# Performance work log

Measured on AMD Instinct MI355X. Metric: run time of the kernel, lower is better.

## Reference

```python
import jax, jax.numpy as jnp
import numpy as np

D_IN = 1024
D_OUT = 1024
NUM_HEADS = 16
HEAD_DIM = D_OUT // NUM_HEADS


def setup_inputs() -> dict:
    key = jax.random.key(0)
    k_x, k_q, k_k, k_v, k_o = jax.random.split(key, 5)
    # Xavier-uniform-ish init for weights (stored as [d_in, d_out] for x @ W)
    lim = float(np.sqrt(6.0 / (D_IN + D_OUT)) / np.sqrt(2.0))
    lim_o = float(np.sqrt(6.0 / (D_OUT + D_OUT)))
    return {
        "x": jax.random.normal(k_x, (2, 2048, D_IN), dtype=jnp.float32),
        "W_query": jax.random.uniform(k_q, (D_IN, D_OUT), jnp.float32, -lim, lim),
        "W_key": jax.random.uniform(k_k, (D_IN, D_OUT), jnp.float32, -lim, lim),
        "W_value": jax.random.uniform(k_v, (D_IN, D_OUT), jnp.float32, -lim, lim),
        "W_out": jax.random.uniform(k_o, (D_OUT, D_OUT), jnp.float32, -lim_o, lim_o),
        "b_out": jnp.zeros((D_OUT,), dtype=jnp.float32),
    }


def reference(x, W_query, W_key, W_value, W_out, b_out):
    B, S, _ = x.shape
    scale = 1.0 / np.sqrt(HEAD_DIM)

    def split_heads(t):  # [B,S,D] -> [B,H,S,hd]
        return t.reshape(B, S, NUM_HEADS, HEAD_DIM).transpose(0, 2, 1, 3)

    q = split_heads(x @ W_query)
    k = split_heads(x @ W_key)
    v = split_heads(x @ W_value)

    scores = jnp.einsum("bhqd,bhkd->bhqk", q, k) * scale  # [B,H,S,S]
    causal = jnp.tril(jnp.ones((S, S), dtype=bool))  # True = keep
    scores = jnp.where(causal, scores, -jnp.inf)
    weights = jax.nn.softmax(scores, axis=-1)
    ctx = jnp.einsum("bhqk,bhkd->bhqd", weights, v)
    ctx = ctx.transpose(0, 2, 1, 3).reshape(B, S, D_OUT)
    return ctx @ W_out + b_out
```

## Files before the change

### kernel.cpp

```cpp
#include <hip/hip_runtime.h>
#include <hip/hip_bf16.h>


typedef __bf16 bf16_t;
typedef __bf16 bf16x4 __attribute__((ext_vector_type(4)));
typedef __bf16 bf16x8 __attribute__((ext_vector_type(8)));
typedef float f32x4 __attribute__((ext_vector_type(4)));

#define AS_GLOBAL __attribute__((address_space(1)))
#define AS_LDS    __attribute__((address_space(3)))

__device__ __forceinline__ void async_load16(const void* g, void* l) {
    __builtin_amdgcn_global_load_lds((AS_GLOBAL void*)(g), (AS_LDS void*)(l), 16, 0, 0);
}

__global__ __launch_bounds__(256) void cvt_f32_bf16(const float* __restrict__ src,
                                                    bf16_t* __restrict__ dst, int n4) {
    int i = blockIdx.x * 256 + threadIdx.x;
    if (i < n4) {
        float4 v = ((const float4*)src)[i];
        bf16x4 o;
        o[0] = (bf16_t)v.x; o[1] = (bf16_t)v.y; o[2] = (bf16_t)v.z; o[3] = (bf16_t)v.w;
        ((bf16x4*)dst)[i] = o;
    }
}

__global__ __launch_bounds__(256) void transpose_cvt4(
    const float* __restrict__ W0, const float* __restrict__ W1,
    const float* __restrict__ W2, const float* __restrict__ W3,
    bf16_t* __restrict__ outbase) {
    __shared__ bf16_t T[64][65];
    int t = threadIdx.x;
    int k0 = blockIdx.x * 64, n0 = blockIdx.y * 64, z = blockIdx.z;
    const float* W = (z == 0) ? W0 : (z == 1) ? W1 : (z == 2) ? W2 : W3;
    bf16_t* WT = outbase + (size_t)z * 1048576;
#pragma unroll
    for (int c = 0; c < 4; c++) {
        int idx = c * 256 + t;
        int row = idx >> 4;
        int col4 = (idx & 15) * 4;
        float4 v = *(const float4*)(W + (k0 + row) * 1024 + n0 + col4);
        T[row][col4 + 0] = (bf16_t)v.x;
        T[row][col4 + 1] = (bf16_t)v.y;
        T[row][col4 + 2] = (bf16_t)v.z;
        T[row][col4 + 3] = (bf16_t)v.w;
    }
    __syncthreads();
#pragma unroll
    for (int c = 0; c < 4; c++) {
        int idx = c * 256 + t;
        int nrow = idx >> 4;
        int kc4 = (idx & 15) * 4;
        bf16x4 o;
        o[0] = T[kc4 + 0][nrow];
        o[1] = T[kc4 + 1][nrow];
        o[2] = T[kc4 + 2][nrow];
        o[3] = T[kc4 + 3][nrow];
        *(bf16x4*)(WT + (n0 + nrow) * 1024 + k0 + kc4) = o;
    }
}

__global__ __launch_bounds__(256) void qkv_gemm(
    const bf16_t* __restrict__ A,
    const bf16_t* __restrict__ WqT, const bf16_t* __restrict__ WkT,
    const bf16_t* __restrict__ WvT,
    bf16_t* __restrict__ Qo, bf16_t* __restrict__ Ko, bf16_t* __restrict__ Vo) {
    const int KD = 1024;
    __shared__ bf16_t As[128 * 32];
    __shared__ bf16_t Bs[128 * 32];
    int tid = threadIdx.x;
    int wave = tid >> 6, lane = tid & 63;
    int quad = lane >> 4, l16 = lane & 15;
    int wm = wave >> 1, wn = wave & 1;
    int z = blockIdx.z;
    const bf16_t* BT = (z == 0) ? WqT : (z == 1) ? WkT : WvT;
    int m0 = blockIdx.x * 128;
    int n0 = blockIdx.y * 128;

    int r = tid >> 2;
    int c8 = (tid & 3) * 8;
    const bf16_t* gA0 = A + (size_t)(m0 + r) * KD + c8;
    const bf16_t* gA1 = A + (size_t)(m0 + 64 + r) * KD + c8;
    const bf16_t* gB0 = BT + (size_t)(n0 + r) * KD + c8;
    const bf16_t* gB1 = BT + (size_t)(n0 + 64 + r) * KD + c8;
    bf16_t* lA0 = As + wave * 512;
    bf16_t* lA1 = As + 2048 + wave * 512;
    bf16_t* lB0 = Bs + wave * 512;
    bf16_t* lB1 = Bs + 2048 + wave * 512;

    f32x4 acc[4][4];
#pragma unroll
    for (int i = 0; i < 4; i++)
#pragma unroll
        for (int j = 0; j < 4; j++) acc[i][j] = (f32x4){0.f, 0.f, 0.f, 0.f};

    for (int k0 = 0; k0 < KD; k0 += 32) {
        async_load16(gA0 + k0, lA0);
        async_load16(gA1 + k0, lA1);
        async_load16(gB0 + k0, lB0);
        async_load16(gB1 + k0, lB1);
        __syncthreads();
        bf16x8 af[4], bfr[4];
#pragma unroll
        for (int mt = 0; mt < 4; mt++)
            af[mt] = *(const bf16x8*)(As + (wm * 64 + mt * 16 + l16) * 32 + quad * 8);
#pragma unroll
        for (int nt = 0; nt < 4; nt++)
            bfr[nt] = *(const bf16x8*)(Bs + (wn * 64 + nt * 16 + l16) * 32 + quad * 8);
        if (z == 2) {
#pragma unroll
            for (int mt = 0; mt < 4; mt++)
#pragma unroll
                for (int nt = 0; nt < 4; nt++)
                    acc[mt][nt] = __builtin_amdgcn_mfma_f32_16x16x32_bf16(
                        bfr[nt], af[mt], acc[mt][nt], 0, 0, 0);
        } else {
#pragma unroll
            for (int mt = 0; mt < 4; mt++)
#pragma unroll
                for (int nt = 0; nt < 4; nt++)
                    acc[mt][nt] = __builtin_amdgcn_mfma_f32_16x16x32_bf16(
                        af[mt], bfr[nt], acc[mt][nt], 0, 0, 0);
        }
        __syncthreads();
    }

    if (z == 0) {
#pragma unroll
        for (int mt = 0; mt < 4; mt++) {
            int mg_base = m0 + wm * 64 + mt * 16 + quad * 4;
#pragma unroll
            for (int nt = 0; nt < 4; nt++) {
                int ng = n0 + wn * 64 + nt * 16 + l16;
                int h = ng >> 6, d = ng & 63;
#pragma unroll
                for (int rr = 0; rr < 4; rr++) {
                    int mg = mg_base + rr;
                    int b = mg >> 11, s = mg & 2047;
                    Qo[(((size_t)(b * 16 + h) * 2048) + s) * 64 + d] =
                        (bf16_t)acc[mt][nt][rr];
                }
            }
        }
    } else if (z == 1) {
#pragma unroll
        for (int mt = 0; mt < 4; mt++) {
            int mg_base = m0 + wm * 64 + mt * 16 + quad * 4;
#pragma unroll
            for (int nt = 0; nt < 4; nt++) {
                int ng = n0 + wn * 64 + nt * 16 + l16;
                int h = ng >> 6, dd = ng & 63;
#pragma unroll
                for (int rr = 0; rr < 4; rr++) {
                    int mg = mg_base + rr;
                    int b = mg >> 11, sl = mg & 2047;
                    int kt = sl >> 6, row = sl & 63;
                    int cc = (dd >> 3) ^ (row & 7);
                    Ko[(size_t)(b * 16 + h) * 131072 + kt * 4096 + row * 64 +
                       cc * 8 + (dd & 7)] = (bf16_t)acc[mt][nt][rr];
                }
            }
        }
    } else {
#pragma unroll
        for (int mt = 0; mt < 4; mt++) {
            int sg = m0 + wm * 64 + mt * 16 + l16;
            int b = sg >> 11, sl = sg & 2047;
            int kt = sl >> 6, srow = sl & 63;
#pragma unroll
            for (int nt = 0; nt < 4; nt++) {
                int dg_base = n0 + wn * 64 + nt * 16 + quad * 4;
#pragma unroll
                for (int rr = 0; rr < 4; rr++) {
                    int dg = dg_base + rr;
                    int h = dg >> 6, dd = dg & 63;
                    int cc = (srow >> 3) ^ (dd & 7);
                    Vo[(size_t)(b * 16 + h) * 131072 + kt * 4096 + dd * 64 +
                       cc * 8 + (srow & 7)] = (bf16_t)acc[mt][nt][rr];
                }
            }
        }
    }
}

__device__ __forceinline__ float exp_pwrite(f32x4 sc[4], bf16_t* Ps,
                                            int wave, int quad, int l16) {
    float part = 0.f;
    int rowbase = (wave * 16 + l16) * 64;
    int gran = (quad & 1) * 4;
    int chi = quad >> 1;
#pragma unroll
    for (int nt = 0; nt < 4; nt++) {
        f32x4 p;
#pragma unroll
        for (int rr = 0; rr < 4; rr++) {
            p[rr] = __builtin_amdgcn_exp2f(sc[nt][rr]);
            part += p[rr];
        }
        bf16x4 pb;
#pragma unroll
        for (int rr = 0; rr < 4; rr++) pb[rr] = (bf16_t)p[rr];
        int cc = (nt * 2 + chi) ^ (l16 & 7);
        *(bf16x4*)(Ps + rowbase + cc * 8 + gran) = pb;
    }
    part += __shfl_xor(part, 16);
    part += __shfl_xor(part, 32);
    return part;
}

__global__ __launch_bounds__(256) void attn(
    const bf16_t* __restrict__ Q, const bf16_t* __restrict__ Kt,
    const bf16_t* __restrict__ Vt, bf16_t* __restrict__ ctx) {
    const int S = 2048;
    __shared__ bf16_t Ks[2][4096];
    __shared__ bf16_t Vs[2][4096];
    __shared__ bf16_t Psa[4096];
    __shared__ bf16_t Psb[4096];
    int tid = threadIdx.x, wave = tid >> 6, lane = tid & 63;
    int quad = lane >> 4, l16 = lane & 15;

    int f = blockIdx.x + 16 * (blockIdx.y + 16 * blockIdx.z);
    int xcd = f & 7, slot = f >> 3;
    int qa = (xcd & 1) * 8 + (slot & 7);
    int bh = (xcd >> 1) + 4 * (slot >> 3);
    int qb = 31 - qa;
    int h = bh & 15, b = bh >> 4;

    const bf16_t* Qbh = Q + (size_t)bh * S * 64;
    const bf16_t* Kbh = Kt + (size_t)bh * 131072;
    const bf16_t* Vbh = Vt + (size_t)bh * 131072;

    const float qs = 0.125f * 1.44269504f;
    bf16x8 aQa[2], aQb[2];
    {
        const bf16_t* ra = Qbh + (size_t)(qa * 64 + wave * 16 + l16) * 64;
        const bf16_t* rb = Qbh + (size_t)(qb * 64 + wave * 16 + l16) * 64;
#pragma unroll
        for (int ks = 0; ks < 2; ks++) {
            bf16x8 ta = *(const bf16x8*)(ra + ks * 32 + quad * 8);
            bf16x8 tb = *(const bf16x8*)(rb + ks * 32 + quad * 8);
#pragma unroll
            for (int j = 0; j < 8; j++) {
                ta[j] = (bf16_t)((float)ta[j] * qs);
                tb[j] = (bf16_t)((float)tb[j] * qs);
            }
            aQa[ks] = ta;
            aQb[ks] = tb;
        }
    }

    float La = 0.f, Lb = 0.f;
    f32x4 Oa[4], Ob[4];
#pragma unroll
    for (int i = 0; i < 4; i++) {
        Oa[i] = (f32x4){0.f, 0.f, 0.f, 0.f};
        Ob[i] = (f32x4){0.f, 0.f, 0.f, 0.f};
    }

    {
        const bf16_t* kg = Kbh + tid * 8;
        const bf16_t* vg = Vbh + tid * 8;
        async_load16(kg, Ks[0] + wave * 512);
        async_load16(kg + 2048, Ks[0] + 2048 + wave * 512);
        async_load16(vg, Vs[0] + wave * 512);
        async_load16(vg + 2048, Vs[0] + 2048 + wave * 512);
    }
    __syncthreads();

    for (int kt = 0; kt <= qb; kt++) {
        int cur = kt & 1;
        if (kt < qb) {
            const bf16_t* kg = Kbh + (kt + 1) * 4096 + tid * 8;
            const bf16_t* vg = Vbh + (kt + 1) * 4096 + tid * 8;
            async_load16(kg, Ks[cur ^ 1] + wave * 512);
            async_load16(kg + 2048, Ks[cur ^ 1] + 2048 + wave * 512);
            async_load16(vg, Vs[cur ^ 1] + wave * 512);
            async_load16(vg + 2048, Vs[cur ^ 1] + 2048 + wave * 512);
        }
        bool dual = (kt <= qa);

        bf16x8 kf[4][2], vf[4][2];
#pragma unroll
        for (int nt = 0; nt < 4; nt++) {
            const bf16_t* krow = Ks[cur] + (nt * 16 + l16) * 64;
            const bf16_t* vrow = Vs[cur] + (nt * 16 + l16) * 64;
#pragma unroll
            for (int ks = 0; ks < 2; ks++) {
                int csw = ((ks * 4 + quad) ^ (l16 & 7)) * 8;
                kf[nt][ks] = *(const bf16x8*)(krow + csw);
                vf[nt][ks] = *(const bf16x8*)(vrow + csw);
            }
        }

        f32x4 sb[4], sa[4];
#pragma unroll
        for (int nt = 0; nt < 4; nt++) {
            f32x4 s = (f32x4){0.f, 0.f, 0.f, 0.f};
            s = __builtin_amdgcn_mfma_f32_16x16x32_bf16(kf[nt][0], aQb[0], s, 0, 0, 0);
            s = __builtin_amdgcn_mfma_f32_16x16x32_bf16(kf[nt][1], aQb[1], s, 0, 0, 0);
            sb[nt] = s;
            if (dual) {
                f32x4 t = (f32x4){0.f, 0.f, 0.f, 0.f};
                t = __builtin_amdgcn_mfma_f32_16x16x32_bf16(kf[nt][0], aQa[0], t, 0, 0, 0);
                t = __builtin_amdgcn_mfma_f32_16x16x32_bf16(kf[nt][1], aQa[1], t, 0, 0, 0);
                sa[nt] = t;
            }
        }
        if (kt == qb) {
            int qg = qb * 64 + wave * 16 + l16;
#pragma unroll
            for (int nt = 0; nt < 4; nt++)
#pragma unroll
                for (int rr = 0; rr < 4; rr++)
                    if (kt * 64 + nt * 16 + quad * 4 + rr > qg) sb[nt][rr] = -1e30f;
        }
        Lb += exp_pwrite(sb, Psb, wave, quad, l16);
        if (dual) {
            if (kt == qa) {
                int qg = qa * 64 + wave * 16 + l16;
#pragma unroll
                for (int nt = 0; nt < 4; nt++)
#pragma unroll
                    for (int rr = 0; rr < 4; rr++)
                        if (kt * 64 + nt * 16 + quad * 4 + rr > qg) sa[nt][rr] = -1e30f;
            }
            La += exp_pwrite(sa, Psa, wave, quad, l16);
        }

#pragma unroll
        for (int ks = 0; ks < 2; ks++) {
            int csw = ((ks * 4 + quad) ^ (l16 & 7)) * 8;
            bf16x8 aPb = *(const bf16x8*)(Psb + (wave * 16 + l16) * 64 + csw);
            bf16x8 aPa;
            if (dual) aPa = *(const bf16x8*)(Psa + (wave * 16 + l16) * 64 + csw);
#pragma unroll
            for (int nt = 0; nt < 4; nt++) {
                Ob[nt] = __builtin_amdgcn_mfma_f32_16x16x32_bf16(aPb, vf[nt][ks],
                                                                 Ob[nt], 0, 0, 0);
                if (dual)
                    Oa[nt] = __builtin_amdgcn_mfma_f32_16x16x32_bf16(aPa, vf[nt][ks],
                                                                     Oa[nt], 0, 0, 0);
            }
        }
        __syncthreads();
    }

    float ila[4], ilb[4];
#pragma unroll
    for (int rr = 0; rr < 4; rr++) {
        ila[rr] = 1.f / __shfl(La, quad * 4 + rr);
        ilb[rr] = 1.f / __shfl(Lb, quad * 4 + rr);
    }
#pragma unroll
    for (int nt = 0; nt < 4; nt++) {
#pragma unroll
        for (int rr = 0; rr < 4; rr++) {
            int qoff = wave * 16 + quad * 4 + rr;
            int col = h * 64 + nt * 16 + l16;
            ctx[(size_t)(b * 2048 + qa * 64 + qoff) * 1024 + col] =
                (bf16_t)(Oa[nt][rr] * ila[rr]);
            ctx[(size_t)(b * 2048 + qb * 64 + qoff) * 1024 + col] =
                (bf16_t)(Ob[nt][rr] * ilb[rr]);
        }
    }
}

__global__ __launch_bounds__(256) void out_gemm(
    const bf16_t* __restrict__ A, const bf16_t* __restrict__ BT,
    const float* __restrict__ bias, float* __restrict__ Cout) {
    const int KD = 1024;
    __shared__ bf16_t As[128 * 32];
    __shared__ bf16_t Bs[128 * 32];
    int tid = threadIdx.x;
    int wave = tid >> 6, lane = tid & 63;
    int quad = lane >> 4, l16 = lane & 15;
    int wm = wave >> 1, wn = wave & 1;
    int m0 = blockIdx.x * 128;
    int n0 = blockIdx.y * 128;

    int r = tid >> 2;
    int c8 = (tid & 3) * 8;
    const bf16_t* gA0 = A + (size_t)(m0 + r) * KD + c8;
    const bf16_t* gA1 = A + (size_t)(m0 + 64 + r) * KD + c8;
    const bf16_t* gB0 = BT + (size_t)(n0 + r) * KD + c8;
    const bf16_t* gB1 = BT + (size_t)(n0 + 64 + r) * KD + c8;
    bf16_t* lA0 = As + wave * 512;
    bf16_t* lA1 = As + 2048 + wave * 512;
    bf16_t* lB0 = Bs + wave * 512;
    bf16_t* lB1 = Bs + 2048 + wave * 512;

    f32x4 acc[4][4];
#pragma unroll
    for (int i = 0; i < 4; i++)
#pragma unroll
        for (int j = 0; j < 4; j++) acc[i][j] = (f32x4){0.f, 0.f, 0.f, 0.f};

    for (int k0 = 0; k0 < KD; k0 += 32) {
        async_load16(gA0 + k0, lA0);
        async_load16(gA1 + k0, lA1);
        async_load16(gB0 + k0, lB0);
        async_load16(gB1 + k0, lB1);
        __syncthreads();
        bf16x8 af[4], bfr[4];
#pragma unroll
        for (int mt = 0; mt < 4; mt++)
            af[mt] = *(const bf16x8*)(As + (wm * 64 + mt * 16 + l16) * 32 + quad * 8);
#pragma unroll
        for (int nt = 0; nt < 4; nt++)
            bfr[nt] = *(const bf16x8*)(Bs + (wn * 64 + nt * 16 + l16) * 32 + quad * 8);
#pragma unroll
        for (int mt = 0; mt < 4; mt++)
#pragma unroll
            for (int nt = 0; nt < 4; nt++)
                acc[mt][nt] = __builtin_amdgcn_mfma_f32_16x16x32_bf16(af[mt], bfr[nt],
                                                                      acc[mt][nt], 0, 0, 0);
        __syncthreads();
    }

#pragma unroll
    for (int mt = 0; mt < 4; mt++) {
        int mg_base = m0 + wm * 64 + mt * 16 + quad * 4;
#pragma unroll
        for (int nt = 0; nt < 4; nt++) {
            int ng = n0 + wn * 64 + nt * 16 + l16;
            float bv = bias[ng];
#pragma unroll
            for (int rr = 0; rr < 4; rr++) {
                int mg = mg_base + rr;
                Cout[(size_t)mg * 1024 + ng] = acc[mt][nt][rr] + bv;
            }
        }
    }
}

extern "C" void kernel_launch(void* const* d_in, const int* in_sizes, int n_in,
                              void* d_out, int out_size, void* d_ws, size_t ws_size,
                              hipStream_t stream) {
    const float* x  = (const float*)d_in[0];
    const float* Wq = (const float*)d_in[1];
    const float* Wk = (const float*)d_in[2];
    const float* Wv = (const float*)d_in[3];
    const float* Wo = (const float*)d_in[4];
    const float* bo = (const float*)d_in[5];
    float* out = (float*)d_out;
    char* ws = (char*)d_ws;

    bf16_t* xb   = (bf16_t*)(ws);
    bf16_t* WTs  = (bf16_t*)(ws + (8u << 20));
    bf16_t* WqT  = WTs;
    bf16_t* WkT  = WTs + 1048576;
    bf16_t* WvT  = WTs + 2097152;
    bf16_t* WoT  = WTs + 3145728;
    bf16_t* Qb   = (bf16_t*)(ws + (16u << 20));
    bf16_t* Kb   = (bf16_t*)(ws + (24u << 20));
    bf16_t* Vb   = (bf16_t*)(ws + (32u << 20));
    bf16_t* ctxb = (bf16_t*)(ws + (40u << 20));

    cvt_f32_bf16<<<4096, 256, 0, stream>>>(x, xb, (4096 * 1024) / 4);
    transpose_cvt4<<<dim3(16, 16, 4), 256, 0, stream>>>(Wq, Wk, Wv, Wo, WTs);
    qkv_gemm<<<dim3(32, 8, 3), 256, 0, stream>>>(xb, WqT, WkT, WvT, Qb, Kb, Vb);
    attn<<<dim3(16, 16, 2), 256, 0, stream>>>(Qb, Kb, Vb, ctxb);
    out_gemm<<<dim3(32, 8), 256, 0, stream>>>(ctxb, WoT, bo, out);
}
```

Before: 214.8 us.

## Double-buffer LDS tiles and XOR-swizzle layout in QKV and output GEMMs

Both GEMM kernels now use two LDS buffers per operand. The next K-tile's async global-to-LDS load is issued before the MFMAs on the current tile, aiming to overlap memory latency with compute and drop one barrier per iteration. The column chunk each thread loads is XOR-swizzled by row, and the fragment reads apply the matching swizzle to reduce LDS bank conflicts. LDS use doubles, which may lower occupancy.

```diff
diff --git a/kernel.cpp b/kernel.cpp
--- a/kernel.cpp
+++ b/kernel.cpp
@@ -66,8 +66,8 @@
     const bf16_t* __restrict__ WvT,
     bf16_t* __restrict__ Qo, bf16_t* __restrict__ Ko, bf16_t* __restrict__ Vo) {
     const int KD = 1024;
-    __shared__ bf16_t As[128 * 32];
-    __shared__ bf16_t Bs[128 * 32];
+    __shared__ bf16_t As[2][128 * 32];
+    __shared__ bf16_t Bs[2][128 * 32];
     int tid = threadIdx.x;
     int wave = tid >> 6, lane = tid & 63;
     int quad = lane >> 4, l16 = lane & 15;
@@ -78,15 +78,11 @@
     int n0 = blockIdx.y * 128;
 
     int r = tid >> 2;
-    int c8 = (tid & 3) * 8;
+    int c8 = (((tid & 3) ^ ((tid >> 3) & 3))) * 8;
     const bf16_t* gA0 = A + (size_t)(m0 + r) * KD + c8;
     const bf16_t* gA1 = A + (size_t)(m0 + 64 + r) * KD + c8;
     const bf16_t* gB0 = BT + (size_t)(n0 + r) * KD + c8;
     const bf16_t* gB1 = BT + (size_t)(n0 + 64 + r) * KD + c8;
-    bf16_t* lA0 = As + wave * 512;
-    bf16_t* lA1 = As + 2048 + wave * 512;
-    bf16_t* lB0 = Bs + wave * 512;
-    bf16_t* lB1 = Bs + 2048 + wave * 512;
 
     f32x4 acc[4][4];
 #pragma unroll
@@ -94,19 +90,29 @@
 #pragma unroll
         for (int j = 0; j < 4; j++) acc[i][j] = (f32x4){0.f, 0.f, 0.f, 0.f};
 
-    for (int k0 = 0; k0 < KD; k0 += 32) {
-        async_load16(gA0 + k0, lA0);
-        async_load16(gA1 + k0, lA1);
-        async_load16(gB0 + k0, lB0);
-        async_load16(gB1 + k0, lB1);
-        __syncthreads();
+    async_load16(gA0, As[0] + wave * 512);
+    async_load16(gA1, As[0] + 2048 + wave * 512);
+    async_load16(gB0, Bs[0] + wave * 512);
+    async_load16(gB1, Bs[0] + 2048 + wave * 512);
+    __syncthreads();
+
+    for (int kk = 0; kk < 32; kk++) {
+        int cur = kk & 1;
+        if (kk < 31) {
+            int k0 = (kk + 1) * 32;
+            async_load16(gA0 + k0, As[cur ^ 1] + wave * 512);
+            async_load16(gA1 + k0, As[cur ^ 1] + 2048 + wave * 512);
+            async_load16(gB0 + k0, Bs[cur ^ 1] + wave * 512);
+            async_load16(gB1 + k0, Bs[cur ^ 1] + 2048 + wave * 512);
+        }
         bf16x8 af[4], bfr[4];
+        int csw = (quad ^ ((l16 >> 1) & 3)) * 8;
 #pragma unroll
         for (int mt = 0; mt < 4; mt++)
-            af[mt] = *(const bf16x8*)(As + (wm * 64 + mt * 16 + l16) * 32 + quad * 8);
+            af[mt] = *(const bf16x8*)(As[cur] + (wm * 64 + mt * 16 + l16) * 32 + csw);
 #pragma unroll
         for (int nt = 0; nt < 4; nt++)
-            bfr[nt] = *(const bf16x8*)(Bs + (wn * 64 + nt * 16 + l16) * 32 + quad * 8);
+            bfr[nt] = *(const bf16x8*)(Bs[cur] + (wn * 64 + nt * 16 + l16) * 32 + csw);
         if (z == 2) {
 #pragma unroll
             for (int mt = 0; mt < 4; mt++)
@@ -369,8 +375,8 @@
     const bf16_t* __restrict__ A, const bf16_t* __restrict__ BT,
     const float* __restrict__ bias, float* __restrict__ Cout) {
     const int KD = 1024;
-    __shared__ bf16_t As[128 * 32];
-    __shared__ bf16_t Bs[128 * 32];
+    __shared__ bf16_t As[2][128 * 32];
+    __shared__ bf16_t Bs[2][128 * 32];
     int tid = threadIdx.x;
     int wave = tid >> 6, lane = tid & 63;
     int quad = lane >> 4, l16 = lane & 15;
@@ -379,15 +385,11 @@
     int n0 = blockIdx.y * 128;
 
     int r = tid >> 2;
-    int c8 = (tid & 3) * 8;
+    int c8 = (((tid & 3) ^ ((tid >> 3) & 3))) * 8;
     const bf16_t* gA0 = A + (size_t)(m0 + r) * KD + c8;
     const bf16_t* gA1 = A + (size_t)(m0 + 64 + r) * KD + c8;
     const bf16_t* gB0 = BT + (size_t)(n0 + r) * KD + c8;
     const bf16_t* gB1 = BT + (size_t)(n0 + 64 + r) * KD + c8;
-    bf16_t* lA0 = As + wave * 512;
-    bf16_t* lA1 = As + 2048 + wave * 512;
-    bf16_t* lB0 = Bs + wave * 512;
-    bf16_t* lB1 = Bs + 2048 + wave * 512;
 
     f32x4 acc[4][4];
 #pragma unroll
@@ -395,19 +397,29 @@
 #pragma unroll
         for (int j = 0; j < 4; j++) acc[i][j] = (f32x4){0.f, 0.f, 0.f, 0.f};
 
-    for (int k0 = 0; k0 < KD; k0 += 32) {
-        async_load16(gA0 + k0, lA0);
-        async_load16(gA1 + k0, lA1);
-        async_load16(gB0 + k0, lB0);
-        async_load16(gB1 + k0, lB1);
-        __syncthreads();
+    async_load16(gA0, As[0] + wave * 512);
+    async_load16(gA1, As[0] + 2048 + wave * 512);
+    async_load16(gB0, Bs[0] + wave * 512);
+    async_load16(gB1, Bs[0] + 2048 + wave * 512);
+    __syncthreads();
+
+    for (int kk = 0; kk < 32; kk++) {
+        int cur = kk & 1;
+        if (kk < 31) {
+            int k0 = (kk + 1) * 32;
+            async_load16(gA0 + k0, As[cur ^ 1] + wave * 512);
+            async_load16(gA1 + k0, As[cur ^ 1] + 2048 + wave * 512);
+            async_load16(gB0 + k0, Bs[cur ^ 1] + wave * 512);
+            async_load16(gB1 + k0, Bs[cur ^ 1] + 2048 + wave * 512);
+        }
         bf16x8 af[4], bfr[4];
+        int csw = (quad ^ ((l16 >> 1) & 3)) * 8;
 #pragma unroll
         for (int mt = 0; mt < 4; mt++)
-            af[mt] = *(const bf16x8*)(As + (wm * 64 + mt * 16 + l16) * 32 + quad * 8);
+            af[mt] = *(const bf16x8*)(As[cur] + (wm * 64 + mt * 16 + l16) * 32 + csw);
 #pragma unroll
         for (int nt = 0; nt < 4; nt++)
-            bfr[nt] = *(const bf16x8*)(Bs + (wn * 64 + nt * 16 + l16) * 32 + quad * 8);
+            bfr[nt] = *(const bf16x8*)(Bs[cur] + (wn * 64 + nt * 16 + l16) * 32 + csw);
 #pragma unroll
         for (int mt = 0; mt < 4; mt++)
 #pragma unroll
```

Result: slower. 227.7 us (+6.0%).
